# Optimization experiments

Measured on AMD Instinct MI355X. Metric: run time of the kernel, lower is better.

Reference implementation:

```python
import jax, jax.numpy as jnp
import numpy as np

B, C, P, L = 16, 64, 128, 16        # batch, channels, patches, patch_length
D = 256                              # d_model / inner_dim
NPF = 256                            # num_poly_feats
NRFF = 128                           # num_rff
RFF_SCALE = 1.0
POLY_DEGREES = (2, 3)                # degree used is poly_degrees[i] - 2 -> (0, 1)
FEAT_DIM = L + NRFF + NPF * len(POLY_DEGREES)  # 16 + 128 + 512 = 656


def setup_inputs() -> dict:
    key = jax.random.key(0)
    ks = jax.random.split(key, 8)
    x = jax.random.normal(ks[0], (B, C, P, L), jnp.float32)
    # nn.Linear weights are (out_features, in_features); stacked over the 2 degrees
    Wq = jax.random.normal(ks[1], (2, D, L), jnp.float32) * 0.1
    Wk = jax.random.normal(ks[2], (2, D, L), jnp.float32) * 0.1
    Wv = jax.random.normal(ks[3], (2, NPF, L), jnp.float32) * 0.1
    freq_w = RFF_SCALE * jax.random.normal(ks[4], (L, NRFF // 2), jnp.float32)
    freq_b = jax.random.normal(ks[5], (1, 1, 1, NRFF // 2), jnp.float32)
    proj_w = jax.random.normal(ks[6], (D, FEAT_DIM), jnp.float32) * 0.02
    proj_b = jax.random.normal(ks[7], (D,), jnp.float32) * 0.02
    return {"x": x, "Wq": Wq, "Wk": Wk, "Wv": Wv,
            "freq_w": freq_w, "freq_b": freq_b,
            "proj_w": proj_w, "proj_b": proj_b}


def reference(x, Wq, Wk, Wv, freq_w, freq_b, proj_w, proj_b):
    # x: (B, C, P, L) -> transpose(1,2): attention runs over the channel axis
    xt = jnp.transpose(x, (0, 2, 1, 3))  # (B, P, C, L)
    polys = []
    for i, deg in enumerate((0, 1)):     # poly_degrees[i] - 2
        xp = xt ** deg                   # deg 0 -> ones, deg 1 -> xt
        Q = jnp.einsum('bpcl,dl->bpcd', xp, Wq[i])   # (B,P,C,D)
        K = jnp.einsum('bpcl,dl->bpcd', xt, Wk[i])   # (B,P,C,D)
        V = jnp.einsum('bpcl,fl->bpcf', xt, Wv[i])   # (B,P,C,NPF)
        S = jnp.einsum('bpcd,bped->bpce', Q, K)      # (B,P,C,C) un-normalized scores
        pf = jnp.einsum('bpce,bpef->bpcf', S, V)     # (B,P,C,NPF)
        polys.append(jnp.transpose(pf, (0, 2, 1, 3)))  # back to (B,C,P,NPF)
    polyfeats = jnp.concatenate(polys, axis=-1)      # (B,C,P,2*NPF)

    wx = x @ freq_w + freq_b                          # (B,C,P,NRFF//2)
    rff = jnp.concatenate([jnp.sin(wx), jnp.cos(wx)], axis=-1)  # (B,C,P,NRFF)

    feats = jnp.concatenate([x, polyfeats, rff], axis=-1)  # (B,C,P,FEAT_DIM)
    return feats @ proj_w.T + proj_b                        # (B,C,P,D)
```

## Files before the change

kernel.cpp:

```cpp
#include <hip/hip_runtime.h>
#include <hip/hip_bf16.h>

#define WS_WK0   0
#define WS_A     16
#define WS_E0    272
#define WS_BT    4368

typedef float f32x4 __attribute__((ext_vector_type(4)));
typedef short s16x8 __attribute__((ext_vector_type(8)));
typedef short s16x4 __attribute__((ext_vector_type(4)));

static __device__ __forceinline__ short bf16b(float f) {
  __hip_bfloat16 h = __float2bfloat16(f);
  return __builtin_bit_cast(short, h);
}
static __device__ __forceinline__ float bf2f(short s) {
  unsigned u = ((unsigned)(unsigned short)s) << 16;
  return __builtin_bit_cast(float, u);
}

static __device__ __forceinline__ void bar_lds() {
  asm volatile("s_waitcnt lgkmcnt(0)\n\ts_barrier" ::: "memory");
}

__global__ __launch_bounds__(512)
void pre_kernel(const float* __restrict__ Wq, const float* __restrict__ Wk,
                const float* __restrict__ Wv, const float* __restrict__ pw,
                float* __restrict__ ws)
{
  __shared__ float lds[8704];
  const int t = threadIdx.x;
  const int blk = blockIdx.x;
  ushort* bt = (ushort*)(ws + WS_BT);

  if (blk == 0) {
    {
      const int d = t >> 1;
      const int lb = (t & 1) * 8;
      #pragma unroll
      for (int h = 0; h < 2; ++h) {
        const float4 vq = *(const float4*)(Wq + 4096 + t*8 + h*4);
        lds[(lb+h*4+0)*256 + d] = vq.x;
        lds[(lb+h*4+1)*256 + d] = vq.y;
        lds[(lb+h*4+2)*256 + d] = vq.z;
        lds[(lb+h*4+3)*256 + d] = vq.w;
        const float4 vk = *(const float4*)(Wk + 4096 + t*8 + h*4);
        lds[4096 + (lb+h*4+0)*256 + d] = vk.x;
        lds[4096 + (lb+h*4+1)*256 + d] = vk.y;
        lds[4096 + (lb+h*4+2)*256 + d] = vk.z;
        lds[4096 + (lb+h*4+3)*256 + d] = vk.w;
      }
    }
    if (t < 256) {
      float s = 0.f;
      #pragma unroll
      for (int q = 0; q < 4; ++q) {
        const float4 v = *(const float4*)(Wq + t*16 + q*4);
        s += v.x + v.y + v.z + v.w;
      }
      lds[8192 + t] = s;
    }
    __syncthreads();
    if (t < 256) {
      const int l1 = t >> 4, l2 = t & 15;
      const float* r1 = lds + l1*256;
      const float* r2 = lds + 4096 + l2*256;
      float s = 0.f;
      #pragma unroll 8
      for (int dq = 0; dq < 64; ++dq) {
        const float4 a = *(const float4*)(r1 + dq*4);
        const float4 b = *(const float4*)(r2 + dq*4);
        s += a.x*b.x + a.y*b.y + a.z*b.z + a.w*b.w;
      }
      ws[WS_A + t] = s;
    }
    if (t < 256) {
      const int l = t & 15, ch = t >> 4;
      float s = 0.f;
      #pragma unroll
      for (int i = 0; i < 16; ++i)
        s += lds[8192 + ch*16 + i] * Wk[(ch*16 + i)*16 + l];
      lds[8448 + t] = s;
    }
    __syncthreads();
    if (t < 16) {
      float s = 0.f;
      #pragma unroll
      for (int ch = 0; ch < 16; ++ch) s += lds[8448 + ch*16 + t];
      ws[WS_WK0 + t] = s;
    }
  } else if (blk <= 16) {
    const int deg = (blk <= 8) ? 0 : 1;
    {
      const int f = t >> 1;
      const int lb = (t & 1) * 8;
      #pragma unroll
      for (int h = 0; h < 2; ++h) {
        const float4 v = *(const float4*)(Wv + deg*4096 + t*8 + h*4);
        lds[(lb+h*4+0)*256 + f] = v.x;
        lds[(lb+h*4+1)*256 + f] = v.y;
        lds[(lb+h*4+2)*256 + f] = v.z;
        lds[(lb+h*4+3)*256 + f] = v.w;
      }
    }
    __syncthreads();
    const int d = ((blk-1) & 7)*32 + (t >> 4);
    const int l = t & 15;
    const float* pr = pw + d*656 + (deg ? 272 : 16);
    const float* wv = lds + l*256;
    float s = 0.f;
    #pragma unroll 8
    for (int fq = 0; fq < 64; ++fq) {
      const float4 a = *(const float4*)(pr + fq*4);
      const float4 b = *(const float4*)(wv + fq*4);
      s += a.x*b.x + a.y*b.y + a.z*b.z + a.w*b.w;
    }
    if (deg == 0) {
      ws[WS_E0 + d*16 + l] = s;
      bt[d*160 + l] = (ushort)bf16b(pw[d*656 + l]);
    } else {
      bt[d*160 + 16 + l] = (ushort)bf16b(s);
    }
  } else {
    #pragma unroll 4
    for (int k = 0; k < 64; ++k) {
      const int d = k*4 + (t >> 7);
      const int j = t & 127;
      const float v = (j < 64) ? pw[d*656 + 528 + j] : pw[d*656 + 592 + (j-64)];
      bt[d*160 + 32 + j] = (ushort)bf16b(v);
    }
  }
}

__global__ __launch_bounds__(256, 2)
void main_kernel(const float* __restrict__ x, const float* __restrict__ fw,
                 const float* __restrict__ fb, const float* __restrict__ pb,
                 const float* __restrict__ ws, float* __restrict__ out)
{
  __shared__ short Xb[64*40];
  __shared__ short XbT[16*72];
  __shared__ short Fwt[64*40];
  __shared__ float fbs[64];
  __shared__ float Gs[256];
  __shared__ float AGs[256];
  __shared__ float tls[16];
  __shared__ float c0s[256];
  __shared__ short Abf[20*64*8];

  const int t = threadIdx.x;
  const int b = blockIdx.x >> 7;
  const int p = blockIdx.x & 127;

  const int lane = t & 63, w = t >> 6;
  const int n0 = w << 6;
  const int lr = lane & 15, lq = lane >> 4;
  const int xc = t >> 2, xl0 = (t & 3) * 4;
  const ushort* BTW = (const ushort*)(ws + WS_BT);

  {
    const float4 v = *(const float4*)(x + (((b*64 + xc)*128 + p) << 4) + xl0);
    s16x4 xb;
    xb[0] = bf16b(v.x); xb[1] = bf16b(v.y); xb[2] = bf16b(v.z); xb[3] = bf16b(v.w);
    s16x4 z; z[0] = 0; z[1] = 0; z[2] = 0; z[3] = 0;
    *(s16x4*)&Xb[xc*40 + xl0] = xb;
    *(s16x4*)&Xb[xc*40 + 16 + xl0] = z;
    XbT[(xl0+0)*72 + xc] = xb[0];
    XbT[(xl0+1)*72 + xc] = xb[1];
    XbT[(xl0+2)*72 + xc] = xb[2];
    XbT[(xl0+3)*72 + xc] = xb[3];
    *(s16x4*)&Abf[(((xl0>>3)*64 + xc) << 3) + (xl0 & 4)] = xb;
    const int l = t >> 4, j0 = (t & 15) * 4;
    const float4 f = *(const float4*)(fw + l*64 + j0);
    Fwt[(j0+0)*40 + l] = (short)bf16b(f.x);
    Fwt[(j0+1)*40 + l] = (short)bf16b(f.y);
    Fwt[(j0+2)*40 + l] = (short)bf16b(f.z);
    Fwt[(j0+3)*40 + l] = (short)bf16b(f.w);
    *(s16x4*)&Fwt[(t>>2)*40 + 16 + (t & 3)*4] = z;
    if (t < 16) *(float4*)(fbs + t*4) = *(const float4*)(fb + t*4);
  }
  bar_lds();

  if (w == 0) {
    f32x4 g = {};
    #pragma unroll
    for (int ks = 0; ks < 2; ++ks) {
      const s16x8 xa = *(const s16x8*)&XbT[lr*72 + ks*32 + lq*8];
      g = __builtin_amdgcn_mfma_f32_16x16x32_bf16(xa, xa, g, 0, 0, 0);
    }
    #pragma unroll
    for (int r = 0; r < 4; ++r) Gs[(lq*4 + r)*16 + lr] = g[r];
  }
  {
    s16x8 xa[4];
    #pragma unroll
    for (int mi = 0; mi < 4; ++mi)
      xa[mi] = *(const s16x8*)&Xb[(mi*16 + lr)*40 + lq*8];
    const s16x8 fwf = *(const s16x8*)&Fwt[(w*16 + lr)*40 + lq*8];
    f32x4 wa[4];
    #pragma unroll
    for (int mi = 0; mi < 4; ++mi) {
      f32x4 zz = {};
      wa[mi] = __builtin_amdgcn_mfma_f32_16x16x32_bf16(xa[mi], fwf, zz, 0, 0, 0);
    }
    const float fbj = fbs[w*16 + lr];
    const int ktS = 4 + 2*w + (lr >> 3);
    const int ktC = ktS + 8;
    const int e = lr & 7;
    #pragma unroll
    for (int mi = 0; mi < 4; ++mi) {
      #pragma unroll
      for (int r = 0; r < 4; ++r) {
        const int c = mi*16 + lq*4 + r;
        float sv, cv;
        __sincosf(wa[mi][r] + fbj, &sv, &cv);
        Abf[(ktS*64 + c)*8 + e] = bf16b(sv);
        Abf[(ktC*64 + c)*8 + e] = bf16b(cv);
      }
    }
  }
  bar_lds();

  {
    const int l = t >> 4, lp = t & 15;
    float a[16];
    #pragma unroll
    for (int q = 0; q < 4; ++q)
      *(float4*)(a + q*4) = *(const float4*)(ws + WS_A + l*16 + q*4);
    float s = 0.f;
    #pragma unroll
    for (int k = 0; k < 16; ++k) s += a[k] * Gs[k*16 + lp];
    AGs[t] = s;
  }
  if (t < 16) {
    float s = 0.f;
    #pragma unroll
    for (int q = 0; q < 4; ++q) {
      const float4 g = *(const float4*)(Gs + t*16 + q*4);
      const float4 wk = *(const float4*)(ws + WS_WK0 + q*4);
      s += g.x*wk.x + g.y*wk.y + g.z*wk.z + g.w*wk.w;
    }
    tls[t] = s;
  }
  bar_lds();

  {
    const s16x8 xlo = *(const s16x8*)&Xb[xc*40];
    const s16x8 xhi = *(const s16x8*)&Xb[xc*40 + 8];
    float4 m = make_float4(0.f, 0.f, 0.f, 0.f);
    #pragma unroll
    for (int i = 0; i < 8; ++i) {
      const float xv = bf2f(xlo[i]);
      const float4 g = *(const float4*)(AGs + i*16 + xl0);
      m.x += xv*g.x; m.y += xv*g.y; m.z += xv*g.z; m.w += xv*g.w;
    }
    #pragma unroll
    for (int i = 0; i < 8; ++i) {
      const float xv = bf2f(xhi[i]);
      const float4 g = *(const float4*)(AGs + (8+i)*16 + xl0);
      m.x += xv*g.x; m.y += xv*g.y; m.z += xv*g.z; m.w += xv*g.w;
    }
    s16x4 mb;
    mb[0] = bf16b(m.x); mb[1] = bf16b(m.y); mb[2] = bf16b(m.z); mb[3] = bf16b(m.w);
    *(s16x4*)&Abf[(((2 + (xl0>>3))*64 + xc) << 3) + (xl0 & 4)] = mb;
  }
  {
    float tl[16], e[16];
    #pragma unroll
    for (int q = 0; q < 4; ++q) {
      *(float4*)(tl + q*4) = *(const float4*)(tls + q*4);
      *(float4*)(e + q*4) = *(const float4*)(ws + WS_E0 + t*16 + q*4);
    }
    float s = pb[t];
    #pragma unroll
    for (int l = 0; l < 16; ++l) s += tl[l] * e[l];
    c0s[t] = s;
  }
  bar_lds();

  f32x4 acc[4][4] = {};
  #pragma unroll
  for (int ks = 0; ks < 5; ++ks) {
    s16x8 af[4], bf_[4];
    #pragma unroll
    for (int mi = 0; mi < 4; ++mi)
      af[mi] = *(const s16x8*)&Abf[(((ks*4 + lq)*64) + mi*16 + lr) << 3];
    #pragma unroll
    for (int nt = 0; nt < 4; ++nt)
      bf_[nt] = *(const s16x8*)&BTW[(n0 + nt*16 + lr)*160 + ks*32 + lq*8];
    #pragma unroll
    for (int mi = 0; mi < 4; ++mi)
      #pragma unroll
      for (int nt = 0; nt < 4; ++nt)
        acc[mi][nt] = __builtin_amdgcn_mfma_f32_16x16x32_bf16(af[mi], bf_[nt], acc[mi][nt], 0, 0, 0);
  }

  #pragma unroll
  for (int nt = 0; nt < 4; ++nt) {
    const int d = n0 + nt*16 + lr;
    const float cc = c0s[d];
    #pragma unroll
    for (int mi = 0; mi < 4; ++mi) {
      #pragma unroll
      for (int r = 0; r < 4; ++r) {
        const int c = mi*16 + lq*4 + r;
        out[(((b*64 + c)*128 + p) << 8) + d] = acc[mi][nt][r] + cc;
      }
    }
  }
}

extern "C" void kernel_launch(void* const* d_in, const int* in_sizes, int n_in,
                              void* d_out, int out_size, void* d_ws, size_t ws_size,
                              hipStream_t stream) {
  const float* x  = (const float*)d_in[0];
  const float* Wq = (const float*)d_in[1];
  const float* Wk = (const float*)d_in[2];
  const float* Wv = (const float*)d_in[3];
  const float* fw = (const float*)d_in[4];
  const float* fb = (const float*)d_in[5];
  const float* pw = (const float*)d_in[6];
  const float* pb = (const float*)d_in[7];
  float* out = (float*)d_out;
  float* ws  = (float*)d_ws;

  pre_kernel<<<18, 512, 0, stream>>>(Wq, Wk, Wv, pw, ws);
  main_kernel<<<16*128, 256, 0, stream>>>(x, fw, fb, pb, ws, out);
}
```

Measured before the change: 51.79 us.

## Split each (b,p) block into two channel halves to double grid size

Doubles the grid so each block handles 32 of the 64 channels for one (batch, patch) pair. The per-block MFMA work, RFF sin/cos, and the Abf LDS tile are halved, and accumulator registers drop from 16 to 8 tiles. This raises parallelism and may improve occupancy. In exchange, each block still loads the full x tile and recomputes the Gram matrix, AG product and bias terms, so that shared prologue work is duplicated.

```diff
diff --git a/kernel.cpp b/kernel.cpp
--- a/kernel.cpp
+++ b/kernel.cpp
@@ -145,11 +145,13 @@
   __shared__ float AGs[256];
   __shared__ float tls[16];
   __shared__ float c0s[256];
-  __shared__ short Abf[20*64*8];
+  __shared__ short Abf[20*32*8];
 
   const int t = threadIdx.x;
-  const int b = blockIdx.x >> 7;
-  const int p = blockIdx.x & 127;
+  const int b  = blockIdx.x >> 8;
+  const int p  = (blockIdx.x >> 1) & 127;
+  const int ch = blockIdx.x & 1;
+  const int c_base = ch << 5;
 
   const int lane = t & 63, w = t >> 6;
   const int n0 = w << 6;
@@ -168,7 +170,8 @@
     XbT[(xl0+1)*72 + xc] = xb[1];
     XbT[(xl0+2)*72 + xc] = xb[2];
     XbT[(xl0+3)*72 + xc] = xb[3];
-    *(s16x4*)&Abf[(((xl0>>3)*64 + xc) << 3) + (xl0 & 4)] = xb;
+    if ((xc >> 5) == ch)
+      *(s16x4*)&Abf[(((xl0>>3)*32 + (xc & 31)) << 3) + (xl0 & 4)] = xb;
     const int l = t >> 4, j0 = (t & 15) * 4;
     const float4 f = *(const float4*)(fw + l*64 + j0);
     Fwt[(j0+0)*40 + l] = (short)bf16b(f.x);
@@ -191,14 +194,14 @@
     for (int r = 0; r < 4; ++r) Gs[(lq*4 + r)*16 + lr] = g[r];
   }
   {
-    s16x8 xa[4];
-    #pragma unroll
-    for (int mi = 0; mi < 4; ++mi)
-      xa[mi] = *(const s16x8*)&Xb[(mi*16 + lr)*40 + lq*8];
+    s16x8 xa[2];
+    #pragma unroll
+    for (int mi = 0; mi < 2; ++mi)
+      xa[mi] = *(const s16x8*)&Xb[(c_base + mi*16 + lr)*40 + lq*8];
     const s16x8 fwf = *(const s16x8*)&Fwt[(w*16 + lr)*40 + lq*8];
-    f32x4 wa[4];
-    #pragma unroll
-    for (int mi = 0; mi < 4; ++mi) {
+    f32x4 wa[2];
+    #pragma unroll
+    for (int mi = 0; mi < 2; ++mi) {
       f32x4 zz = {};
       wa[mi] = __builtin_amdgcn_mfma_f32_16x16x32_bf16(xa[mi], fwf, zz, 0, 0, 0);
     }
@@ -207,14 +210,14 @@
     const int ktC = ktS + 8;
     const int e = lr & 7;
     #pragma unroll
-    for (int mi = 0; mi < 4; ++mi) {
+    for (int mi = 0; mi < 2; ++mi) {
       #pragma unroll
       for (int r = 0; r < 4; ++r) {
-        const int c = mi*16 + lq*4 + r;
+        const int cl = mi*16 + lq*4 + r;
         float sv, cv;
         __sincosf(wa[mi][r] + fbj, &sv, &cv);
-        Abf[(ktS*64 + c)*8 + e] = bf16b(sv);
-        Abf[(ktC*64 + c)*8 + e] = bf16b(cv);
+        Abf[(ktS*32 + cl)*8 + e] = bf16b(sv);
+        Abf[(ktC*32 + cl)*8 + e] = bf16b(cv);
       }
     }
   }
@@ -243,25 +246,27 @@
   }
   bar_lds();
 
-  {
-    const s16x8 xlo = *(const s16x8*)&Xb[xc*40];
-    const s16x8 xhi = *(const s16x8*)&Xb[xc*40 + 8];
+  if (t < 128) {
+    const int cl = t >> 2, lp0 = (t & 3) * 4;
+    const int c = c_base + cl;
+    const s16x8 xlo = *(const s16x8*)&Xb[c*40];
+    const s16x8 xhi = *(const s16x8*)&Xb[c*40 + 8];
     float4 m = make_float4(0.f, 0.f, 0.f, 0.f);
     #pragma unroll
     for (int i = 0; i < 8; ++i) {
       const float xv = bf2f(xlo[i]);
-      const float4 g = *(const float4*)(AGs + i*16 + xl0);
+      const float4 g = *(const float4*)(AGs + i*16 + lp0);
       m.x += xv*g.x; m.y += xv*g.y; m.z += xv*g.z; m.w += xv*g.w;
     }
     #pragma unroll
     for (int i = 0; i < 8; ++i) {
       const float xv = bf2f(xhi[i]);
-      const float4 g = *(const float4*)(AGs + (8+i)*16 + xl0);
+      const float4 g = *(const float4*)(AGs + (8+i)*16 + lp0);
       m.x += xv*g.x; m.y += xv*g.y; m.z += xv*g.z; m.w += xv*g.w;
     }
     s16x4 mb;
     mb[0] = bf16b(m.x); mb[1] = bf16b(m.y); mb[2] = bf16b(m.z); mb[3] = bf16b(m.w);
-    *(s16x4*)&Abf[(((2 + (xl0>>3))*64 + xc) << 3) + (xl0 & 4)] = mb;
+    *(s16x4*)&Abf[(((2 + (lp0>>3))*32 + cl) << 3) + (lp0 & 4)] = mb;
   }
   {
     float tl[16], e[16];
@@ -277,18 +282,18 @@
   }
   bar_lds();
 
-  f32x4 acc[4][4] = {};
+  f32x4 acc[2][4] = {};
   #pragma unroll
   for (int ks = 0; ks < 5; ++ks) {
-    s16x8 af[4], bf_[4];
-    #pragma unroll
-    for (int mi = 0; mi < 4; ++mi)
-      af[mi] = *(const s16x8*)&Abf[(((ks*4 + lq)*64) + mi*16 + lr) << 3];
+    s16x8 af[2], bf_[4];
+    #pragma unroll
+    for (int mi = 0; mi < 2; ++mi)
+      af[mi] = *(const s16x8*)&Abf[(((ks*4 + lq)*32) + mi*16 + lr) << 3];
     #pragma unroll
     for (int nt = 0; nt < 4; ++nt)
       bf_[nt] = *(const s16x8*)&BTW[(n0 + nt*16 + lr)*160 + ks*32 + lq*8];
     #pragma unroll
-    for (int mi = 0; mi < 4; ++mi)
+    for (int mi = 0; mi < 2; ++mi)
       #pragma unroll
       for (int nt = 0; nt < 4; ++nt)
         acc[mi][nt] = __builtin_amdgcn_mfma_f32_16x16x32_bf16(af[mi], bf_[nt], acc[mi][nt], 0, 0, 0);
@@ -299,10 +304,10 @@
     const int d = n0 + nt*16 + lr;
     const float cc = c0s[d];
     #pragma unroll
-    for (int mi = 0; mi < 4; ++mi) {
+    for (int mi = 0; mi < 2; ++mi) {
       #pragma unroll
       for (int r = 0; r < 4; ++r) {
-        const int c = mi*16 + lq*4 + r;
+        const int c = c_base + mi*16 + lq*4 + r;
         out[(((b*64 + c)*128 + p) << 8) + d] = acc[mi][nt][r] + cc;
       }
     }
@@ -324,5 +329,5 @@
   float* ws  = (float*)d_ws;
 
   pre_kernel<<<18, 512, 0, stream>>>(Wq, Wk, Wv, pw, ws);
-  main_kernel<<<16*128, 256, 0, stream>>>(x, fw, fb, pb, ws, out);
-}
+  main_kernel<<<16*128*2, 256, 0, stream>>>(x, fw, fb, pb, ws, out);
+}
```

New measurement: 62.28 us. 1.2x slower.

## Compute Gram products redundantly per wave with MFMA and drop block barriers

Applied to the files above, without the earlier changes.

Each wave now computes its own copy of the 16x16 Gram matrix and the A·G product into per-wave LDS buffers. This lets two block-wide barriers be replaced with wave-local LDS waits. The scalar FMA loops for A·G and X·AG are replaced with bf16 MFMA calls. The frequency-weight and A fragments are loaded directly from global into registers instead of going through a transposed LDS staging buffer. In exchange, the intermediates A·G and AG are rounded to bf16 rather than kept in fp32, which lowers accuracy, and the small MFMA work is duplicated across all four waves.

```diff
diff --git a/kernel.cpp b/kernel.cpp
--- a/kernel.cpp
+++ b/kernel.cpp
@@ -14,13 +14,12 @@
   __hip_bfloat16 h = __float2bfloat16(f);
   return __builtin_bit_cast(short, h);
 }
-static __device__ __forceinline__ float bf2f(short s) {
-  unsigned u = ((unsigned)(unsigned short)s) << 16;
-  return __builtin_bit_cast(float, u);
-}
 
 static __device__ __forceinline__ void bar_lds() {
   asm volatile("s_waitcnt lgkmcnt(0)\n\ts_barrier" ::: "memory");
+}
+static __device__ __forceinline__ void fence_lds() {
+  asm volatile("s_waitcnt lgkmcnt(0)" ::: "memory");
 }
 
 __global__ __launch_bounds__(512)
@@ -139,11 +138,10 @@
 {
   __shared__ short Xb[64*40];
   __shared__ short XbT[16*72];
-  __shared__ short Fwt[64*40];
   __shared__ float fbs[64];
-  __shared__ float Gs[256];
-  __shared__ float AGs[256];
-  __shared__ float tls[16];
+  __shared__ float Gs[4][256];
+  __shared__ float AGs[4][256];
+  __shared__ float tls_s[16];
   __shared__ float c0s[256];
   __shared__ short Abf[20*64*8];
 
@@ -169,33 +167,32 @@
     XbT[(xl0+2)*72 + xc] = xb[2];
     XbT[(xl0+3)*72 + xc] = xb[3];
     *(s16x4*)&Abf[(((xl0>>3)*64 + xc) << 3) + (xl0 & 4)] = xb;
-    const int l = t >> 4, j0 = (t & 15) * 4;
-    const float4 f = *(const float4*)(fw + l*64 + j0);
-    Fwt[(j0+0)*40 + l] = (short)bf16b(f.x);
-    Fwt[(j0+1)*40 + l] = (short)bf16b(f.y);
-    Fwt[(j0+2)*40 + l] = (short)bf16b(f.z);
-    Fwt[(j0+3)*40 + l] = (short)bf16b(f.w);
-    *(s16x4*)&Fwt[(t>>2)*40 + 16 + (t & 3)*4] = z;
     if (t < 16) *(float4*)(fbs + t*4) = *(const float4*)(fb + t*4);
   }
+  s16x8 aconst, fwf;
+  #pragma unroll
+  for (int e = 0; e < 8; ++e) {
+    aconst[e] = (lq < 2) ? bf16b(ws[WS_A + lr*16 + lq*8 + e]) : (short)0;
+    fwf[e]    = (lq < 2) ? bf16b(fw[(lq*8 + e)*64 + w*16 + lr]) : (short)0;
+  }
   bar_lds();
 
-  if (w == 0) {
+  {
     f32x4 g = {};
     #pragma unroll
     for (int ks = 0; ks < 2; ++ks) {
-      const s16x8 xa = *(const s16x8*)&XbT[lr*72 + ks*32 + lq*8];
-      g = __builtin_amdgcn_mfma_f32_16x16x32_bf16(xa, xa, g, 0, 0, 0);
-    }
-    #pragma unroll
-    for (int r = 0; r < 4; ++r) Gs[(lq*4 + r)*16 + lr] = g[r];
-  }
-  {
-    s16x8 xa[4];
-    #pragma unroll
-    for (int mi = 0; mi < 4; ++mi)
-      xa[mi] = *(const s16x8*)&Xb[(mi*16 + lr)*40 + lq*8];
-    const s16x8 fwf = *(const s16x8*)&Fwt[(w*16 + lr)*40 + lq*8];
+      const s16x8 xt = *(const s16x8*)&XbT[lr*72 + ks*32 + lq*8];
+      g = __builtin_amdgcn_mfma_f32_16x16x32_bf16(xt, xt, g, 0, 0, 0);
+    }
+    #pragma unroll
+    for (int r = 0; r < 4; ++r) Gs[w][(lq*4 + r)*16 + lr] = g[r];
+  }
+
+  s16x8 xa[4];
+  #pragma unroll
+  for (int mi = 0; mi < 4; ++mi)
+    xa[mi] = *(const s16x8*)&Xb[(mi*16 + lr)*40 + lq*8];
+  {
     f32x4 wa[4];
     #pragma unroll
     for (int mi = 0; mi < 4; ++mi) {
@@ -218,56 +215,53 @@
       }
     }
   }
-  bar_lds();
-
-  {
-    const int l = t >> 4, lp = t & 15;
-    float a[16];
-    #pragma unroll
-    for (int q = 0; q < 4; ++q)
-      *(float4*)(a + q*4) = *(const float4*)(ws + WS_A + l*16 + q*4);
+
+  fence_lds();
+
+  {
+    s16x8 gfrag;
+    #pragma unroll
+    for (int e = 0; e < 8; ++e)
+      gfrag[e] = (lq < 2) ? bf16b(Gs[w][(lq*8 + e)*16 + lr]) : (short)0;
+    f32x4 zz = {};
+    const f32x4 agv = __builtin_amdgcn_mfma_f32_16x16x32_bf16(aconst, gfrag, zz, 0, 0, 0);
+    #pragma unroll
+    for (int r = 0; r < 4; ++r) AGs[w][(lq*4 + r)*16 + lr] = agv[r];
+  }
+  if (lq == 0) {
     float s = 0.f;
     #pragma unroll
-    for (int k = 0; k < 16; ++k) s += a[k] * Gs[k*16 + lp];
-    AGs[t] = s;
-  }
-  if (t < 16) {
-    float s = 0.f;
-    #pragma unroll
     for (int q = 0; q < 4; ++q) {
-      const float4 g = *(const float4*)(Gs + t*16 + q*4);
-      const float4 wk = *(const float4*)(ws + WS_WK0 + q*4);
-      s += g.x*wk.x + g.y*wk.y + g.z*wk.z + g.w*wk.w;
-    }
-    tls[t] = s;
-  }
-  bar_lds();
-
-  {
-    const s16x8 xlo = *(const s16x8*)&Xb[xc*40];
-    const s16x8 xhi = *(const s16x8*)&Xb[xc*40 + 8];
-    float4 m = make_float4(0.f, 0.f, 0.f, 0.f);
-    #pragma unroll
-    for (int i = 0; i < 8; ++i) {
-      const float xv = bf2f(xlo[i]);
-      const float4 g = *(const float4*)(AGs + i*16 + xl0);
-      m.x += xv*g.x; m.y += xv*g.y; m.z += xv*g.z; m.w += xv*g.w;
-    }
-    #pragma unroll
-    for (int i = 0; i < 8; ++i) {
-      const float xv = bf2f(xhi[i]);
-      const float4 g = *(const float4*)(AGs + (8+i)*16 + xl0);
-      m.x += xv*g.x; m.y += xv*g.y; m.z += xv*g.z; m.w += xv*g.w;
-    }
-    s16x4 mb;
-    mb[0] = bf16b(m.x); mb[1] = bf16b(m.y); mb[2] = bf16b(m.z); mb[3] = bf16b(m.w);
-    *(s16x4*)&Abf[(((2 + (xl0>>3))*64 + xc) << 3) + (xl0 & 4)] = mb;
+      const float4 gq = *(const float4*)&Gs[w][lr*16 + q*4];
+      const float4 wkq = *(const float4*)(ws + WS_WK0 + q*4);
+      s += gq.x*wkq.x + gq.y*wkq.y + gq.z*wkq.z + gq.w*wkq.w;
+    }
+    tls_s[lr] = s;
+  }
+
+  fence_lds();
+
+  {
+    s16x8 agfrag;
+    #pragma unroll
+    for (int e = 0; e < 8; ++e)
+      agfrag[e] = (lq < 2) ? bf16b(AGs[w][(lq*8 + e)*16 + lr]) : (short)0;
+    #pragma unroll
+    for (int mi = 0; mi < 4; ++mi) {
+      f32x4 zz = {};
+      const f32x4 m = __builtin_amdgcn_mfma_f32_16x16x32_bf16(xa[mi], agfrag, zz, 0, 0, 0);
+      #pragma unroll
+      for (int r = 0; r < 4; ++r) {
+        const int c = mi*16 + lq*4 + r;
+        Abf[((2 + (lr >> 3))*64 + c)*8 + (lr & 7)] = bf16b(m[r]);
+      }
+    }
   }
   {
     float tl[16], e[16];
     #pragma unroll
     for (int q = 0; q < 4; ++q) {
-      *(float4*)(tl + q*4) = *(const float4*)(tls + q*4);
+      *(float4*)(tl + q*4) = *(const float4*)(tls_s + q*4);
       *(float4*)(e + q*4) = *(const float4*)(ws + WS_E0 + t*16 + q*4);
     }
     float s = pb[t];
```

Result: slower. 64.83 us (+25.2%).

## Split fused main kernel into activation-builder and GEMM kernels via workspace

Applied to the files above, without the earlier changes.

Moves the per-(b,p) feature building (bf16 conversion, RFF sincos, polynomial terms, bias constant) into a separate acts_kernel that writes the bf16 A-tile and per-block bias to global workspace. A second gemm_kernel then reads these slabs and runs the MFMA projection without LDS. The split is chosen when the workspace is large enough, otherwise the fused kernel is kept. It aims to lower LDS and register pressure in the GEMM, at the cost of an extra launch and a global round trip of about 40 MB of intermediates.

```diff
diff --git a/kernel.cpp b/kernel.cpp
--- a/kernel.cpp
+++ b/kernel.cpp
@@ -5,6 +5,9 @@
 #define WS_A     16
 #define WS_E0    272
 #define WS_BT    4368
+#define WS_C0    24848
+#define WS_ACT   549136
+#define WS_SPLIT_FLOATS (549136 + 2048*5120)
 
 typedef float f32x4 __attribute__((ext_vector_type(4)));
 typedef short s16x8 __attribute__((ext_vector_type(8)));
@@ -18,7 +21,6 @@
   unsigned u = ((unsigned)(unsigned short)s) << 16;
   return __builtin_bit_cast(float, u);
 }
-
 static __device__ __forceinline__ void bar_lds() {
   asm volatile("s_waitcnt lgkmcnt(0)\n\ts_barrier" ::: "memory");
 }
@@ -132,10 +134,115 @@
   }
 }
 
+#define ACTS_PHASES(B_, P_)                                                      \
+  {                                                                              \
+    const float4 v = *(const float4*)(x + (((B_*64 + xc)*128 + P_) << 4) + xl0); \
+    s16x4 xb;                                                                    \
+    xb[0] = bf16b(v.x); xb[1] = bf16b(v.y); xb[2] = bf16b(v.z); xb[3] = bf16b(v.w); \
+    s16x4 z; z[0] = 0; z[1] = 0; z[2] = 0; z[3] = 0;                             \
+    *(s16x4*)&Xb[xc*40 + xl0] = xb;                                              \
+    *(s16x4*)&Xb[xc*40 + 16 + xl0] = z;                                          \
+    XbT[(xl0+0)*72 + xc] = xb[0];                                                \
+    XbT[(xl0+1)*72 + xc] = xb[1];                                                \
+    XbT[(xl0+2)*72 + xc] = xb[2];                                                \
+    XbT[(xl0+3)*72 + xc] = xb[3];                                                \
+    *(s16x4*)&Abf[(((xl0>>3)*64 + xc) << 3) + (xl0 & 4)] = xb;                   \
+    const int l_ = t >> 4, j0_ = (t & 15) * 4;                                   \
+    const float4 f_ = *(const float4*)(fw + l_*64 + j0_);                        \
+    Fwt[(j0_+0)*40 + l_] = (short)bf16b(f_.x);                                   \
+    Fwt[(j0_+1)*40 + l_] = (short)bf16b(f_.y);                                   \
+    Fwt[(j0_+2)*40 + l_] = (short)bf16b(f_.z);                                   \
+    Fwt[(j0_+3)*40 + l_] = (short)bf16b(f_.w);                                   \
+    *(s16x4*)&Fwt[(t>>2)*40 + 16 + (t & 3)*4] = z;                               \
+    if (t < 16) *(float4*)(fbs + t*4) = *(const float4*)(fb + t*4);              \
+  }                                                                              \
+  bar_lds();                                                                     \
+  if (w == 0) {                                                                  \
+    f32x4 g = {};                                                                \
+    _Pragma("unroll")                                                            \
+    for (int ks = 0; ks < 2; ++ks) {                                             \
+      const s16x8 xa_ = *(const s16x8*)&XbT[lr*72 + ks*32 + lq*8];               \
+      g = __builtin_amdgcn_mfma_f32_16x16x32_bf16(xa_, xa_, g, 0, 0, 0);         \
+    }                                                                            \
+    _Pragma("unroll")                                                            \
+    for (int r = 0; r < 4; ++r) Gs[(lq*4 + r)*16 + lr] = g[r];                   \
+  }                                                                              \
+  {                                                                              \
+    s16x8 xa[4];                                                                 \
+    _Pragma("unroll")                                                            \
+    for (int mi = 0; mi < 4; ++mi)                                               \
+      xa[mi] = *(const s16x8*)&Xb[(mi*16 + lr)*40 + lq*8];                       \
+    const s16x8 fwf = *(const s16x8*)&Fwt[(w*16 + lr)*40 + lq*8];                \
+    f32x4 wa[4];                                                                 \
+    _Pragma("unroll")                                                            \
+    for (int mi = 0; mi < 4; ++mi) {                                             \
+      f32x4 zz = {};                                                             \
+      wa[mi] = __builtin_amdgcn_mfma_f32_16x16x32_bf16(xa[mi], fwf, zz, 0, 0, 0);\
+    }                                                                            \
+    const float fbj = fbs[w*16 + lr];                                            \
+    const int ktS = 4 + 2*w + (lr >> 3);                                         \
+    const int ktC = ktS + 8;                                                     \
+    const int e = lr & 7;                                                        \
+    _Pragma("unroll")                                                            \
+    for (int mi = 0; mi < 4; ++mi) {                                             \
+      _Pragma("unroll")                                                          \
+      for (int r = 0; r < 4; ++r) {                                              \
+        const int c = mi*16 + lq*4 + r;                                          \
+        float sv, cv;                                                            \
+        __sincosf(wa[mi][r] + fbj, &sv, &cv);                                    \
+        Abf[(ktS*64 + c)*8 + e] = bf16b(sv);                                     \
+        Abf[(ktC*64 + c)*8 + e] = bf16b(cv);                                     \
+      }                                                                          \
+    }                                                                            \
+  }                                                                              \
+  bar_lds();                                                                     \
+  {                                                                              \
+    const int l_ = t >> 4, lp_ = t & 15;                                         \
+    float a_[16];                                                                \
+    _Pragma("unroll")                                                            \
+    for (int q = 0; q < 4; ++q)                                                  \
+      *(float4*)(a_ + q*4) = *(const float4*)(ws + WS_A + l_*16 + q*4);          \
+    float s_ = 0.f;                                                              \
+    _Pragma("unroll")                                                            \
+    for (int k = 0; k < 16; ++k) s_ += a_[k] * Gs[k*16 + lp_];                   \
+    AGs[t] = s_;                                                                 \
+  }                                                                              \
+  if (t < 16) {                                                                  \
+    float s_ = 0.f;                                                              \
+    _Pragma("unroll")                                                            \
+    for (int q = 0; q < 4; ++q) {                                                \
+      const float4 g_ = *(const float4*)(Gs + t*16 + q*4);                       \
+      const float4 wk_ = *(const float4*)(ws + WS_WK0 + q*4);                    \
+      s_ += g_.x*wk_.x + g_.y*wk_.y + g_.z*wk_.z + g_.w*wk_.w;                   \
+    }                                                                            \
+    tls[t] = s_;                                                                 \
+  }                                                                              \
+  bar_lds();                                                                     \
+  {                                                                              \
+    const s16x8 xlo = *(const s16x8*)&Xb[xc*40];                                 \
+    const s16x8 xhi = *(const s16x8*)&Xb[xc*40 + 8];                             \
+    float4 m = make_float4(0.f, 0.f, 0.f, 0.f);                                  \
+    _Pragma("unroll")                                                            \
+    for (int i = 0; i < 8; ++i) {                                                \
+      const float xv = bf2f(xlo[i]);                                             \
+      const float4 g_ = *(const float4*)(AGs + i*16 + xl0);                      \
+      m.x += xv*g_.x; m.y += xv*g_.y; m.z += xv*g_.z; m.w += xv*g_.w;            \
+    }                                                                            \
+    _Pragma("unroll")                                                            \
+    for (int i = 0; i < 8; ++i) {                                                \
+      const float xv = bf2f(xhi[i]);                                             \
+      const float4 g_ = *(const float4*)(AGs + (8+i)*16 + xl0);                  \
+      m.x += xv*g_.x; m.y += xv*g_.y; m.z += xv*g_.z; m.w += xv*g_.w;            \
+    }                                                                            \
+    s16x4 mb;                                                                    \
+    mb[0] = bf16b(m.x); mb[1] = bf16b(m.y); mb[2] = bf16b(m.z); mb[3] = bf16b(m.w); \
+    *(s16x4*)&Abf[(((2 + (xl0>>3))*64 + xc) << 3) + (xl0 & 4)] = mb;             \
+  }
+
 __global__ __launch_bounds__(256, 2)
-void main_kernel(const float* __restrict__ x, const float* __restrict__ fw,
-                 const float* __restrict__ fb, const float* __restrict__ pb,
-                 const float* __restrict__ ws, float* __restrict__ out)
+void main_fused(const float* __restrict__ x, const float* __restrict__ fw,
+                const float* __restrict__ fb, const float* __restrict__ pb,
+                const float* __restrict__ ws, float* __restrict__ out)
 {
   __shared__ short Xb[64*40];
   __shared__ short XbT[16*72];
@@ -150,119 +257,13 @@
   const int t = threadIdx.x;
   const int b = blockIdx.x >> 7;
   const int p = blockIdx.x & 127;
-
   const int lane = t & 63, w = t >> 6;
   const int n0 = w << 6;
   const int lr = lane & 15, lq = lane >> 4;
   const int xc = t >> 2, xl0 = (t & 3) * 4;
   const ushort* BTW = (const ushort*)(ws + WS_BT);
 
-  {
-    const float4 v = *(const float4*)(x + (((b*64 + xc)*128 + p) << 4) + xl0);
-    s16x4 xb;
-    xb[0] = bf16b(v.x); xb[1] = bf16b(v.y); xb[2] = bf16b(v.z); xb[3] = bf16b(v.w);
-    s16x4 z; z[0] = 0; z[1] = 0; z[2] = 0; z[3] = 0;
-    *(s16x4*)&Xb[xc*40 + xl0] = xb;
-    *(s16x4*)&Xb[xc*40 + 16 + xl0] = z;
-    XbT[(xl0+0)*72 + xc] = xb[0];
-    XbT[(xl0+1)*72 + xc] = xb[1];
-    XbT[(xl0+2)*72 + xc] = xb[2];
-    XbT[(xl0+3)*72 + xc] = xb[3];
-    *(s16x4*)&Abf[(((xl0>>3)*64 + xc) << 3) + (xl0 & 4)] = xb;
-    const int l = t >> 4, j0 = (t & 15) * 4;
-    const float4 f = *(const float4*)(fw + l*64 + j0);
-    Fwt[(j0+0)*40 + l] = (short)bf16b(f.x);
-    Fwt[(j0+1)*40 + l] = (short)bf16b(f.y);
-    Fwt[(j0+2)*40 + l] = (short)bf16b(f.z);
-    Fwt[(j0+3)*40 + l] = (short)bf16b(f.w);
-    *(s16x4*)&Fwt[(t>>2)*40 + 16 + (t & 3)*4] = z;
-    if (t < 16) *(float4*)(fbs + t*4) = *(const float4*)(fb + t*4);
-  }
-  bar_lds();
-
-  if (w == 0) {
-    f32x4 g = {};
-    #pragma unroll
-    for (int ks = 0; ks < 2; ++ks) {
-      const s16x8 xa = *(const s16x8*)&XbT[lr*72 + ks*32 + lq*8];
-      g = __builtin_amdgcn_mfma_f32_16x16x32_bf16(xa, xa, g, 0, 0, 0);
-    }
-    #pragma unroll
-    for (int r = 0; r < 4; ++r) Gs[(lq*4 + r)*16 + lr] = g[r];
-  }
-  {
-    s16x8 xa[4];
-    #pragma unroll
-    for (int mi = 0; mi < 4; ++mi)
-      xa[mi] = *(const s16x8*)&Xb[(mi*16 + lr)*40 + lq*8];
-    const s16x8 fwf = *(const s16x8*)&Fwt[(w*16 + lr)*40 + lq*8];
-    f32x4 wa[4];
-    #pragma unroll
-    for (int mi = 0; mi < 4; ++mi) {
-      f32x4 zz = {};
-      wa[mi] = __builtin_amdgcn_mfma_f32_16x16x32_bf16(xa[mi], fwf, zz, 0, 0, 0);
-    }
-    const float fbj = fbs[w*16 + lr];
-    const int ktS = 4 + 2*w + (lr >> 3);
-    const int ktC = ktS + 8;
-    const int e = lr & 7;
-    #pragma unroll
-    for (int mi = 0; mi < 4; ++mi) {
-      #pragma unroll
-      for (int r = 0; r < 4; ++r) {
-        const int c = mi*16 + lq*4 + r;
-        float sv, cv;
-        __sincosf(wa[mi][r] + fbj, &sv, &cv);
-        Abf[(ktS*64 + c)*8 + e] = bf16b(sv);
-        Abf[(ktC*64 + c)*8 + e] = bf16b(cv);
-      }
-    }
-  }
-  bar_lds();
-
-  {
-    const int l = t >> 4, lp = t & 15;
-    float a[16];
-    #pragma unroll
-    for (int q = 0; q < 4; ++q)
-      *(float4*)(a + q*4) = *(const float4*)(ws + WS_A + l*16 + q*4);
-    float s = 0.f;
-    #pragma unroll
-    for (int k = 0; k < 16; ++k) s += a[k] * Gs[k*16 + lp];
-    AGs[t] = s;
-  }
-  if (t < 16) {
-    float s = 0.f;
-    #pragma unroll
-    for (int q = 0; q < 4; ++q) {
-      const float4 g = *(const float4*)(Gs + t*16 + q*4);
-      const float4 wk = *(const float4*)(ws + WS_WK0 + q*4);
-      s += g.x*wk.x + g.y*wk.y + g.z*wk.z + g.w*wk.w;
-    }
-    tls[t] = s;
-  }
-  bar_lds();
-
-  {
-    const s16x8 xlo = *(const s16x8*)&Xb[xc*40];
-    const s16x8 xhi = *(const s16x8*)&Xb[xc*40 + 8];
-    float4 m = make_float4(0.f, 0.f, 0.f, 0.f);
-    #pragma unroll
-    for (int i = 0; i < 8; ++i) {
-      const float xv = bf2f(xlo[i]);
-      const float4 g = *(const float4*)(AGs + i*16 + xl0);
-      m.x += xv*g.x; m.y += xv*g.y; m.z += xv*g.z; m.w += xv*g.w;
-    }
-    #pragma unroll
-    for (int i = 0; i < 8; ++i) {
-      const float xv = bf2f(xhi[i]);
-      const float4 g = *(const float4*)(AGs + (8+i)*16 + xl0);
-      m.x += xv*g.x; m.y += xv*g.y; m.z += xv*g.z; m.w += xv*g.w;
-    }
-    s16x4 mb;
-    mb[0] = bf16b(m.x); mb[1] = bf16b(m.y); mb[2] = bf16b(m.z); mb[3] = bf16b(m.w);
-    *(s16x4*)&Abf[(((2 + (xl0>>3))*64 + xc) << 3) + (xl0 & 4)] = mb;
-  }
+  ACTS_PHASES(b, p)
   {
     float tl[16], e[16];
     #pragma unroll
@@ -293,11 +294,97 @@
       for (int nt = 0; nt < 4; ++nt)
         acc[mi][nt] = __builtin_amdgcn_mfma_f32_16x16x32_bf16(af[mi], bf_[nt], acc[mi][nt], 0, 0, 0);
   }
-
   #pragma unroll
   for (int nt = 0; nt < 4; ++nt) {
     const int d = n0 + nt*16 + lr;
     const float cc = c0s[d];
+    #pragma unroll
+    for (int mi = 0; mi < 4; ++mi) {
+      #pragma unroll
+      for (int r = 0; r < 4; ++r) {
+        const int c = mi*16 + lq*4 + r;
+        out[(((b*64 + c)*128 + p) << 8) + d] = acc[mi][nt][r] + cc;
+      }
+    }
+  }
+}
+
+__global__ __launch_bounds__(256, 2)
+void acts_kernel(const float* __restrict__ x, const float* __restrict__ fw,
+                 const float* __restrict__ fb, const float* __restrict__ pb,
+                 float* __restrict__ ws)
+{
+  __shared__ short Xb[64*40];
+  __shared__ short XbT[16*72];
+  __shared__ short Fwt[64*40];
+  __shared__ float fbs[64];
+  __shared__ float Gs[256];
+  __shared__ float AGs[256];
+  __shared__ float tls[16];
+  __shared__ short Abf[20*64*8];
+
+  const int t = threadIdx.x;
+  const int b = blockIdx.x >> 7;
+  const int p = blockIdx.x & 127;
+  const int lane = t & 63, w = t >> 6;
+  const int lr = lane & 15, lq = lane >> 4;
+  const int xc = t >> 2, xl0 = (t & 3) * 4;
+
+  ACTS_PHASES(b, p)
+  {
+    float tl[16], e[16];
+    #pragma unroll
+    for (int q = 0; q < 4; ++q) {
+      *(float4*)(tl + q*4) = *(const float4*)(tls + q*4);
+      *(float4*)(e + q*4) = *(const float4*)(ws + WS_E0 + t*16 + q*4);
+    }
+    float s = pb[t];
+    #pragma unroll
+    for (int l = 0; l < 16; ++l) s += tl[l] * e[l];
+    ws[WS_C0 + (size_t)blockIdx.x*256 + t] = s;
+  }
+  bar_lds();
+
+  ushort* so = (ushort*)(ws + WS_ACT) + (size_t)blockIdx.x * 10240;
+  #pragma unroll
+  for (int q = 0; q < 5; ++q)
+    *(s16x8*)&so[q*2048 + t*8] = *(const s16x8*)&Abf[q*2048 + t*8];
+}
+
+__global__ __launch_bounds__(256, 2)
+void gemm_kernel(const float* __restrict__ ws, float* __restrict__ out)
+{
+  const int t = threadIdx.x;
+  const int bid = blockIdx.x;
+  const int b = bid >> 7;
+  const int p = bid & 127;
+  const int lane = t & 63, w = t >> 6;
+  const int n0 = w << 6;
+  const int lr = lane & 15, lq = lane >> 4;
+  const ushort* BTW = (const ushort*)(ws + WS_BT);
+  const ushort* slab = (const ushort*)(ws + WS_ACT) + (size_t)bid * 10240;
+  const float* C0 = ws + WS_C0 + (size_t)bid * 256;
+
+  f32x4 acc[4][4] = {};
+  #pragma unroll
+  for (int ks = 0; ks < 5; ++ks) {
+    s16x8 af[4], bf_[4];
+    #pragma unroll
+    for (int mi = 0; mi < 4; ++mi)
+      af[mi] = *(const s16x8*)&slab[(((ks*4 + lq)*64) + mi*16 + lr) << 3];
+    #pragma unroll
+    for (int nt = 0; nt < 4; ++nt)
+      bf_[nt] = *(const s16x8*)&BTW[(n0 + nt*16 + lr)*160 + ks*32 + lq*8];
+    #pragma unroll
+    for (int mi = 0; mi < 4; ++mi)
+      #pragma unroll
+      for (int nt = 0; nt < 4; ++nt)
+        acc[mi][nt] = __builtin_amdgcn_mfma_f32_16x16x32_bf16(af[mi], bf_[nt], acc[mi][nt], 0, 0, 0);
+  }
+  #pragma unroll
+  for (int nt = 0; nt < 4; ++nt) {
+    const int d = n0 + nt*16 + lr;
+    const float cc = C0[d];
     #pragma unroll
     for (int mi = 0; mi < 4; ++mi) {
       #pragma unroll
@@ -324,5 +411,10 @@
   float* ws  = (float*)d_ws;
 
   pre_kernel<<<18, 512, 0, stream>>>(Wq, Wk, Wv, pw, ws);
-  main_kernel<<<16*128, 256, 0, stream>>>(x, fw, fb, pb, ws, out);
-}
+  if (ws_size >= (size_t)WS_SPLIT_FLOATS * 4) {
+    acts_kernel<<<16*128, 256, 0, stream>>>(x, fw, fb, pb, ws);
+    gemm_kernel<<<16*128, 256, 0, stream>>>(ws, out);
+  } else {
+    main_fused<<<16*128, 256, 0, stream>>>(x, fw, fb, pb, ws, out);
+  }
+}
```

Measured after the change: 69.09 us. 1.33x slower.
